# Kernel tuning notes

Measured on AMD Instinct MI355X. Metric: run time of the kernel, lower is better.

Reference implementation:

```python
import jax, jax.numpy as jnp
import numpy as np

IN_F = 4096
OUT_F = 4096
BLOCK = 16      # weight values decoded per latent code
D_LAT = 16      # latent dim per code
HID = 64        # decoder hidden width
K = 65536       # codebook size
NB = IN_F * OUT_F // BLOCK  # 1,048,576 blocks


def setup_inputs() -> dict:
    key = jax.random.key(0)
    ks = jax.random.split(key, 10)
    return {
        "x": jax.random.normal(ks[0], (4, 2048, IN_F), jnp.float32),
        "y_in_idx": jax.random.randint(ks[1], (NB,), 0, K),
        "codebook": jax.random.normal(ks[2], (K, D_LAT), jnp.float32) * 0.1,
        "W1": jax.random.normal(ks[3], (D_LAT, HID), jnp.float32) * 0.1,
        "b1": jnp.zeros((HID,), jnp.float32),
        "W2": jax.random.normal(ks[4], (HID, BLOCK), jnp.float32) * 0.1,
        "b2": jnp.zeros((BLOCK,), jnp.float32),
        "scale": jax.random.uniform(ks[5], (OUT_F,), jnp.float32, 0.5, 1.5),
        "shift": jax.random.normal(ks[6], (OUT_F,), jnp.float32) * 0.01,
        "bias": jax.random.normal(ks[7], (OUT_F,), jnp.float32) * 0.02,
    }


def reference(x, y_in_idx, codebook, W1, b1, W2, b2, scale, shift, bias):
    # 1) gather latent codes for every weight block: [NB, D_LAT]
    codes = codebook[y_in_idx]
    # 2) decode latents -> weight blocks via small MLP (comp_W_from_y analogue)
    h = jax.nn.relu(codes @ W1 + b1)          # [NB, HID]
    blocks = h @ W2 + b2                      # [NB, BLOCK]
    # 3) assemble reconstructed (standardized) weight hatWr: [OUT_F, IN_F]
    Wr = blocks.reshape(OUT_F, IN_F)
    # 4) de-standardize with per-output-row metadata (de_standardize_Wr)
    W_hat = Wr * scale[:, None] + shift[:, None]
    # 5) F.linear(input, W_hat, bias): [B, S, OUT_F]
    return jnp.einsum('bsi,oi->bso', x, W_hat) + bias
```

## Files before the change

kernel.cpp:

```cpp
#include <hip/hip_runtime.h>
#include <hip/hip_bf16.h>

#define IN_F   4096
#define OUT_F  4096
#define HID    64
#define D_LAT  16
#define BLK    16
#define NB     (IN_F * OUT_F / BLK)
#define M_TOT  8192
#define K_TOT  IN_F
#define N_TOT  OUT_F

typedef __bf16 bf16x8 __attribute__((ext_vector_type(8)));
typedef float  f32x4  __attribute__((ext_vector_type(4)));

__global__ __launch_bounds__(256) void convert_x_kernel(
    const float* __restrict__ x, __hip_bfloat16* __restrict__ xb) {
  size_t i = ((size_t)blockIdx.x * 256 + threadIdx.x) * 8;
  const float4* p = (const float4*)(x + i);
  float4 a = p[0], b = p[1];
  union { __hip_bfloat16 h[8]; uint4 q; } u;
  u.h[0] = __float2bfloat16(a.x); u.h[1] = __float2bfloat16(a.y);
  u.h[2] = __float2bfloat16(a.z); u.h[3] = __float2bfloat16(a.w);
  u.h[4] = __float2bfloat16(b.x); u.h[5] = __float2bfloat16(b.y);
  u.h[6] = __float2bfloat16(b.z); u.h[7] = __float2bfloat16(b.w);
  *(uint4*)(xb + i) = u.q;
}

__global__ __launch_bounds__(256) void decode_kernel(
    const int* __restrict__ yidx, const float* __restrict__ codebook,
    const float* __restrict__ W1, const float* __restrict__ b1,
    const float* __restrict__ W2, const float* __restrict__ b2,
    const float* __restrict__ scale, const float* __restrict__ shift,
    __hip_bfloat16* __restrict__ What) {
  int t = threadIdx.x;
  int b = blockIdx.x * 256 + t;
  int o = blockIdx.x;
  int id = yidx[b];
  const float4* cb = (const float4*)(codebook + (size_t)id * D_LAT);
  float4 c0 = cb[0], c1 = cb[1], c2 = cb[2], c3 = cb[3];
  float code[16] = {c0.x, c0.y, c0.z, c0.w, c1.x, c1.y, c1.z, c1.w,
                    c2.x, c2.y, c2.z, c2.w, c3.x, c3.y, c3.z, c3.w};
  float h[HID];
#pragma unroll
  for (int j = 0; j < HID; j++) h[j] = b1[j];
#pragma unroll
  for (int d = 0; d < D_LAT; d++) {
    float cd = code[d];
#pragma unroll
    for (int j = 0; j < HID; j++) h[j] = fmaf(cd, W1[d * HID + j], h[j]);
  }
  float acc[BLK];
#pragma unroll
  for (int c = 0; c < BLK; c++) acc[c] = b2[c];
#pragma unroll
  for (int j = 0; j < HID; j++) {
    float hj = fmaxf(h[j], 0.f);
#pragma unroll
    for (int c = 0; c < BLK; c++) acc[c] = fmaf(hj, W2[j * BLK + c], acc[c]);
  }
  float sc = scale[o], sh = shift[o];
  union { __hip_bfloat16 h16[16]; uint4 q[2]; } u;
#pragma unroll
  for (int c = 0; c < BLK; c++) u.h16[c] = __float2bfloat16(fmaf(acc[c], sc, sh));
  uint4* dst = (uint4*)(What + (size_t)b * BLK);
  dst[0] = u.q[0];
  dst[1] = u.q[1];
}

__device__ inline void gload_lds16(const void* g, void* l) {
  __builtin_amdgcn_global_load_lds(
      (const __attribute__((address_space(1))) void*)g,
      (__attribute__((address_space(3))) void*)l, 16, 0, 0);
}

__global__ __launch_bounds__(256, 2) void gemm_bt_kernel(
    const __hip_bfloat16* __restrict__ A, const __hip_bfloat16* __restrict__ B,
    const float* __restrict__ bias, float* __restrict__ C) {
  __shared__ __align__(16) __hip_bfloat16 sA[256 * 32];
  __shared__ __align__(16) __hip_bfloat16 sB[128 * 32];
  const int lane = threadIdx.x & 63;
  const int wave = threadIdx.x >> 6;
  const int m0 = blockIdx.y * 256;
  const int n0 = blockIdx.x * 128;
  const int wr = wave >> 1;
  const int wc = wave & 1;

  const int srow = lane >> 2;
  const int schk = (lane & 3) ^ ((lane >> 3) & 3);
  const __hip_bfloat16* aSrc =
      A + (size_t)(m0 + wave * 64 + srow) * K_TOT + schk * 8;
  const __hip_bfloat16* bSrc =
      B + (size_t)(n0 + wave * 32 + srow) * K_TOT + schk * 8;

  const int fl = lane & 15;
  const int pos = (lane >> 4) ^ ((fl >> 1) & 3);
  const __hip_bfloat16* aRd = &sA[(wr * 128 + fl) * 32 + pos * 8];
  const __hip_bfloat16* bRd = &sB[(wc * 64 + fl) * 32 + pos * 8];

  f32x4 acc[8][4];
#pragma unroll
  for (int i = 0; i < 8; i++)
#pragma unroll
    for (int j = 0; j < 4; j++) acc[i][j] = (f32x4){0.f, 0.f, 0.f, 0.f};

  for (int k0 = 0; k0 < K_TOT; k0 += 32) {
#pragma unroll
    for (int i = 0; i < 4; i++)
      gload_lds16(aSrc + (size_t)i * 16 * K_TOT + k0,
                  (char*)sA + (wave * 4 + i) * 1024);
#pragma unroll
    for (int i = 0; i < 2; i++)
      gload_lds16(bSrc + (size_t)i * 16 * K_TOT + k0,
                  (char*)sB + (wave * 2 + i) * 1024);
    __syncthreads();

    bf16x8 bf[4];
#pragma unroll
    for (int nt = 0; nt < 4; nt++) bf[nt] = *(const bf16x8*)(bRd + nt * 16 * 32);
#pragma unroll
    for (int mt = 0; mt < 8; mt++) {
      bf16x8 af = *(const bf16x8*)(aRd + mt * 16 * 32);
#pragma unroll
      for (int nt = 0; nt < 4; nt++)
        acc[mt][nt] = __builtin_amdgcn_mfma_f32_16x16x32_bf16(
            af, bf[nt], acc[mt][nt], 0, 0, 0);
    }
    __syncthreads();
  }

  float bs[4];
#pragma unroll
  for (int nt = 0; nt < 4; nt++) bs[nt] = bias[n0 + wc * 64 + nt * 16 + fl];
#pragma unroll
  for (int mt = 0; mt < 8; mt++) {
    int r0 = m0 + wr * 128 + mt * 16 + (lane >> 4) * 4;
#pragma unroll
    for (int nt = 0; nt < 4; nt++) {
      int cn = n0 + wc * 64 + nt * 16 + fl;
#pragma unroll
      for (int r = 0; r < 4; r++)
        C[(size_t)(r0 + r) * N_TOT + cn] = acc[mt][nt][r] + bs[nt];
    }
  }
}

extern "C" void kernel_launch(void* const* d_in, const int* in_sizes, int n_in,
                              void* d_out, int out_size, void* d_ws, size_t ws_size,
                              hipStream_t stream) {
  const float* x        = (const float*)d_in[0];
  const int*   yidx     = (const int*)d_in[1];
  const float* codebook = (const float*)d_in[2];
  const float* W1       = (const float*)d_in[3];
  const float* b1       = (const float*)d_in[4];
  const float* W2       = (const float*)d_in[5];
  const float* b2       = (const float*)d_in[6];
  const float* scale    = (const float*)d_in[7];
  const float* shift    = (const float*)d_in[8];
  const float* bias     = (const float*)d_in[9];
  float* out = (float*)d_out;

  __hip_bfloat16* What = (__hip_bfloat16*)d_ws;
  __hip_bfloat16* xb   = (__hip_bfloat16*)((char*)d_ws + (size_t)32 * 1024 * 1024);

  convert_x_kernel<<<(M_TOT * (size_t)K_TOT) / (256 * 8), 256, 0, stream>>>(x, xb);
  decode_kernel<<<NB / 256, 256, 0, stream>>>(yidx, codebook, W1, b1, W2, b2,
                                              scale, shift, What);
  gemm_bt_kernel<<<dim3(N_TOT / 128, M_TOT / 256), 256, 0, stream>>>(xb, What, bias, out);
}
```

Before: 562.9 us.

## Run the latent decoder MLP on MFMA instructions instead of scalar FMAs

Result: faster. 546.5 us (-2.9%).

```diff
diff --git a/kernel.cpp b/kernel.cpp
--- a/kernel.cpp
+++ b/kernel.cpp
@@ -27,45 +27,93 @@
   *(uint4*)(xb + i) = u.q;
 }
 
-__global__ __launch_bounds__(256) void decode_kernel(
+__global__ __launch_bounds__(256) void decode_mfma_kernel(
     const int* __restrict__ yidx, const float* __restrict__ codebook,
     const float* __restrict__ W1, const float* __restrict__ b1,
     const float* __restrict__ W2, const float* __restrict__ b2,
     const float* __restrict__ scale, const float* __restrict__ shift,
     __hip_bfloat16* __restrict__ What) {
-  int t = threadIdx.x;
-  int b = blockIdx.x * 256 + t;
-  int o = blockIdx.x;
-  int id = yidx[b];
-  const float4* cb = (const float4*)(codebook + (size_t)id * D_LAT);
-  float4 c0 = cb[0], c1 = cb[1], c2 = cb[2], c3 = cb[3];
-  float code[16] = {c0.x, c0.y, c0.z, c0.w, c1.x, c1.y, c1.z, c1.w,
-                    c2.x, c2.y, c2.z, c2.w, c3.x, c3.y, c3.z, c3.w};
-  float h[HID];
-#pragma unroll
-  for (int j = 0; j < HID; j++) h[j] = b1[j];
-#pragma unroll
-  for (int d = 0; d < D_LAT; d++) {
-    float cd = code[d];
-#pragma unroll
-    for (int j = 0; j < HID; j++) h[j] = fmaf(cd, W1[d * HID + j], h[j]);
-  }
-  float acc[BLK];
-#pragma unroll
-  for (int c = 0; c < BLK; c++) acc[c] = b2[c];
-#pragma unroll
-  for (int j = 0; j < HID; j++) {
-    float hj = fmaxf(h[j], 0.f);
-#pragma unroll
-    for (int c = 0; c < BLK; c++) acc[c] = fmaf(hj, W2[j * BLK + c], acc[c]);
-  }
-  float sc = scale[o], sh = shift[o];
-  union { __hip_bfloat16 h16[16]; uint4 q[2]; } u;
-#pragma unroll
-  for (int c = 0; c < BLK; c++) u.h16[c] = __float2bfloat16(fmaf(acc[c], sc, sh));
-  uint4* dst = (uint4*)(What + (size_t)b * BLK);
-  dst[0] = u.q[0];
-  dst[1] = u.q[1];
+  __shared__ __align__(16) __hip_bfloat16 sH[4][16 * 72];
+  const int lane = threadIdx.x & 63;
+  const int wave = threadIdx.x >> 6;
+  const int n = lane & 15;
+  const int q = lane >> 4;
+  const bool act = q < 2;
+
+  union { __hip_bfloat16 h[8]; bf16x8 v; } uz;
+#pragma unroll
+  for (int j = 0; j < 8; j++) uz.h[j] = __float2bfloat16(0.f);
+  const bf16x8 zf = uz.v;
+  const f32x4 z4 = (f32x4){0.f, 0.f, 0.f, 0.f};
+
+  bf16x8 frag1[4];
+#pragma unroll
+  for (int g = 0; g < 4; g++) {
+    union { __hip_bfloat16 h[8]; bf16x8 v; } u;
+#pragma unroll
+    for (int j = 0; j < 8; j++) {
+      int k = (q * 8 + j) & 15;
+      float w = act ? W1[k * HID + g * 16 + n] : 0.f;
+      u.h[j] = __float2bfloat16(w);
+    }
+    frag1[g] = u.v;
+  }
+  bf16x8 frag2[2];
+#pragma unroll
+  for (int kk = 0; kk < 2; kk++) {
+    union { __hip_bfloat16 h[8]; bf16x8 v; } u;
+#pragma unroll
+    for (int j = 0; j < 8; j++)
+      u.h[j] = __float2bfloat16(W2[(kk * 32 + q * 8 + j) * BLK + n]);
+    frag2[kk] = u.v;
+  }
+  float b1v[4];
+#pragma unroll
+  for (int g = 0; g < 4; g++) b1v[g] = b1[g * 16 + n];
+  const float b2v = b2[n];
+
+  const int c0w = blockIdx.x * 256 + wave * 64;
+#pragma unroll 1
+  for (int i = 0; i < 4; i++) {
+    const int cbase = c0w + i * 16;
+    const int id = yidx[cbase + n];
+    const float4* cp = (const float4*)(codebook + (size_t)id * D_LAT + (q & 1) * 8);
+    float4 ca = cp[0], cb = cp[1];
+    union { __hip_bfloat16 h[8]; bf16x8 v; } ua;
+    ua.h[0] = __float2bfloat16(ca.x); ua.h[1] = __float2bfloat16(ca.y);
+    ua.h[2] = __float2bfloat16(ca.z); ua.h[3] = __float2bfloat16(ca.w);
+    ua.h[4] = __float2bfloat16(cb.x); ua.h[5] = __float2bfloat16(cb.y);
+    ua.h[6] = __float2bfloat16(cb.z); ua.h[7] = __float2bfloat16(cb.w);
+    bf16x8 afrag = act ? ua.v : zf;
+
+    f32x4 hC[4];
+#pragma unroll
+    for (int g = 0; g < 4; g++)
+      hC[g] = __builtin_amdgcn_mfma_f32_16x16x32_bf16(afrag, frag1[g], z4, 0, 0, 0);
+
+    __syncthreads();
+#pragma unroll
+    for (int g = 0; g < 4; g++)
+#pragma unroll
+      for (int r = 0; r < 4; r++) {
+        float hv = fmaxf(hC[g][r] + b1v[g], 0.f);
+        sH[wave][(q * 4 + r) * 72 + g * 16 + n] = __float2bfloat16(hv);
+      }
+    __syncthreads();
+
+    bf16x8 a2_0 = *(const bf16x8*)&sH[wave][n * 72 + q * 8];
+    bf16x8 a2_1 = *(const bf16x8*)&sH[wave][n * 72 + 32 + q * 8];
+    f32x4 o4 = __builtin_amdgcn_mfma_f32_16x16x32_bf16(a2_0, frag2[0], z4, 0, 0, 0);
+    o4 = __builtin_amdgcn_mfma_f32_16x16x32_bf16(a2_1, frag2[1], o4, 0, 0, 0);
+
+    const int o = cbase >> 8;
+    const float sc = scale[o], sh = shift[o];
+#pragma unroll
+    for (int r = 0; r < 4; r++) {
+      int code = cbase + q * 4 + r;
+      What[(size_t)code * BLK + n] = __float2bfloat16((o4[r] + b2v) * sc + sh);
+    }
+  }
 }
 
 __device__ inline void gload_lds16(const void* g, void* l) {
@@ -164,7 +212,7 @@
   __hip_bfloat16* xb   = (__hip_bfloat16*)((char*)d_ws + (size_t)32 * 1024 * 1024);
 
   convert_x_kernel<<<(M_TOT * (size_t)K_TOT) / (256 * 8), 256, 0, stream>>>(x, xb);
-  decode_kernel<<<NB / 256, 256, 0, stream>>>(yidx, codebook, W1, b1, W2, b2,
-                                              scale, shift, What);
+  decode_mfma_kernel<<<NB / 256, 256, 0, stream>>>(yidx, codebook, W1, b1, W2, b2,
+                                                   scale, shift, What);
   gemm_bt_kernel<<<dim3(N_TOT / 128, M_TOT / 256), 256, 0, stream>>>(xb, What, bias, out);
 }
```
